# Performance work log

Measured on AMD Instinct MI355X. Metric: run time of the kernel, lower is better.

## Reference

```python
import jax, jax.numpy as jnp
import numpy as np

BS, DEG, H = 32, 4, 32
OUT = H  # n_aggr=1 inside Full -> out_size = n_aggr * h_size = h_size


def setup_inputs() -> dict:
    key = jax.random.key(0)
    k1, k2 = jax.random.split(key)
    neighbour_h = jax.random.normal(k1, (BS, DEG, H), dtype=jnp.float32)
    hp1 = H + 1
    t_shape = (hp1,) * DEG + (OUT,)  # [33,33,33,33,32]
    # xavier_uniform-like scale: fan_in = hp1**DEG, fan_out = OUT
    scale = float(np.sqrt(2.0 / (hp1 ** DEG + OUT)))
    T = jax.random.normal(k2, t_shape, dtype=jnp.float32) * scale
    return {"neighbour_h": neighbour_h, "T": T}


def reference(neighbour_h, T):
    # Full.forward: chunk neighbour_h along child dim, feed to AugmentedTensor.
    # AugmentedTensor: sequentially contract T against each child's augmented
    # embedding [h_i ; 1] over the leading axes of T.
    bs, deg, h = neighbour_h.shape
    hp1 = h + 1
    # augment with trailing 1 (bias slot): [bs, deg, h+1]
    h_aug = jnp.concatenate(
        [neighbour_h, jnp.ones((bs, deg, 1), neighbour_h.dtype)], axis=2
    )
    # first contraction: [bs, hp1] @ [hp1, hp1^(deg-1)*out]
    res = jnp.matmul(h_aug[:, 0, :], T.reshape(hp1, -1))
    # remaining contractions shrink the trailing dim by hp1 each step
    for i in range(1, deg):
        res = jnp.einsum("bi,bio->bo", h_aug[:, i, :], res.reshape(bs, hp1, -1))
    return res  # [bs, out_size] == [bs, h_size] since n_aggr=1
```

## Files before the change

### kernel.cpp

```cpp
#include <hip/hip_runtime.h>
#include <hip/hip_bf16.h>

#define HSZ 32
#define HP1 33
#define M3 35937
#define M3P2 35968
#define TI_STRIDE 1149984
#define TIB ((size_t)TI_STRIDE * 4)
#define NBLK 1124
#define NT 64
#define DEPTH 6

#define OFF_A0T   0
#define OFF_D     8192
#define OFF_TILES 4612096

typedef short bf16x8 __attribute__((ext_vector_type(8)));
typedef float f32x16 __attribute__((ext_vector_type(16)));

__device__ inline short f2bf(float f) {
  __hip_bfloat16 h = __float2bfloat16(f);
  return __builtin_bit_cast(short, h);
}

__global__ __launch_bounds__(256) void k_pre(const float* __restrict__ nh,
                                             float* __restrict__ a0T,
                                             float* __restrict__ D,
                                             float* __restrict__ tiles) {
  const int b = blockIdx.y;
  const int m = blockIdx.x * 256 + threadIdx.x;
  if (m < M3P2) {
    float v = 0.f;
    if (m < M3) {
      const int j = m / 1089;
      const int r = m - j * 1089;
      const int k = r / 33;
      const int l = r - k * 33;
      const float a1 = (j < HSZ) ? nh[(b * 4 + 1) * HSZ + j] : 1.0f;
      const float a2 = (k < HSZ) ? nh[(b * 4 + 2) * HSZ + k] : 1.0f;
      const float a3 = (l < HSZ) ? nh[(b * 4 + 3) * HSZ + l] : 1.0f;
      v = a1 * a2 * a3;
    }
    D[(size_t)b * M3P2 + m] = v;
  }
  if (blockIdx.x == 0 && threadIdx.x < HP1) {
    const int i = threadIdx.x;
    a0T[i * 32 + b] = (i < HSZ) ? nh[(b * 4 + 0) * HSZ + i] : 1.0f;
  }
  if (b == 1 && blockIdx.x < 64) {
    ((float4*)tiles)[blockIdx.x * 256 + threadIdx.x] =
        make_float4(0.f, 0.f, 0.f, 0.f);
  }
}

__global__ __launch_bounds__(64) void k_main(const float* __restrict__ T,
                                             const float* __restrict__ a0T,
                                             const float* __restrict__ D,
                                             float* __restrict__ tiles) {
  __shared__ float lds[DEPTH * 1024];
  const int blk = blockIdx.x;
  const int m0 = blk * 32;
  const int l = (int)threadIdx.x;
  const int bo = l & 31;
  const int g = l >> 5;

  const float* dp = D + (size_t)bo * M3P2 + m0 + 8 * g;
  float df0[8], df1[8];
  *(float4*)(df0)     = *(const float4*)(dp);
  *(float4*)(df0 + 4) = *(const float4*)(dp + 4);
  *(float4*)(df1)     = *(const float4*)(dp + 16);
  *(float4*)(df1 + 4) = *(const float4*)(dp + 20);

  float a0v[HP1];
#pragma unroll
  for (int i = 0; i < HP1; ++i) a0v[i] = a0T[i * 32 + bo];

  {
    float s = 0.f;
#pragma unroll
    for (int e = 0; e < 8; ++e) s += df0[e] + df1[e];
#pragma unroll
    for (int i = 0; i < HP1; ++i) s += a0v[i];
    asm volatile("" :: "v"(s) : "memory");
  }

  const int mrel = l >> 3;
  size_t src[4];
#pragma unroll
  for (int q = 0; q < 4; ++q) {
    const bool valid = (m0 + 8 * q + mrel) < M3;
    src[q] = valid ? ((size_t)(m0 * 32 + q * 256 + l * 4) * 4) : 0;
  }
  const char* Tb = (const char*)T;

#define ISSUE(row_, slot_)                                                    \
  {                                                                           \
    _Pragma("unroll")                                                         \
    for (int q = 0; q < 4; ++q) {                                             \
      __builtin_amdgcn_global_load_lds(                                       \
          (const __attribute__((address_space(1))) void*)(                    \
              Tb + (size_t)(row_)*TIB + src[q]),                              \
          (__attribute__((address_space(3))) void*)(                          \
              &lds[(slot_)*1024 + q * 256]),                                  \
          16, 0, 0);                                                          \
    }                                                                         \
  }

  ISSUE(0, 0) ISSUE(1, 1) ISSUE(2, 2) ISSUE(3, 3) ISSUE(4, 4) ISSUE(5, 5)

  f32x16 acc = {};

#define STEP(i_, vm_, doIssue_)                                               \
  {                                                                           \
    asm volatile("s_waitcnt vmcnt(" #vm_ ")" ::: "memory");                   \
    __builtin_amdgcn_sched_barrier(0);                                        \
    float tv0[8], tv1[8];                                                     \
    _Pragma("unroll")                                                         \
    for (int e = 0; e < 8; ++e) {                                             \
      tv0[e] = lds[((i_) % DEPTH) * 1024 + (8 * g + e) * 32 + bo];            \
      tv1[e] = lds[((i_) % DEPTH) * 1024 + 512 + (8 * g + e) * 32 + bo];      \
    }                                                                         \
    asm volatile("s_waitcnt lgkmcnt(0)" ::: "memory");                        \
    if (doIssue_) ISSUE((i_) + DEPTH, (i_) % DEPTH)                           \
    bf16x8 af0, bf0, af1, bf1;                                                \
    _Pragma("unroll")                                                         \
    for (int e = 0; e < 8; ++e) {                                             \
      af0[e] = f2bf(a0v[i_] * df0[e]);                                        \
      bf0[e] = f2bf(tv0[e]);                                                  \
      af1[e] = f2bf(a0v[i_] * df1[e]);                                        \
      bf1[e] = f2bf(tv1[e]);                                                  \
    }                                                                         \
    acc = __builtin_amdgcn_mfma_f32_32x32x16_bf16(af0, bf0, acc, 0, 0, 0);    \
    acc = __builtin_amdgcn_mfma_f32_32x32x16_bf16(af1, bf1, acc, 0, 0, 0);    \
  }

  STEP(0, 20, 1)  STEP(1, 20, 1)  STEP(2, 20, 1)  STEP(3, 20, 1)
  STEP(4, 20, 1)  STEP(5, 20, 1)  STEP(6, 20, 1)  STEP(7, 20, 1)
  STEP(8, 20, 1)  STEP(9, 20, 1)  STEP(10, 20, 1) STEP(11, 20, 1)
  STEP(12, 20, 1) STEP(13, 20, 1) STEP(14, 20, 1) STEP(15, 20, 1)
  STEP(16, 20, 1) STEP(17, 20, 1) STEP(18, 20, 1) STEP(19, 20, 1)
  STEP(20, 20, 1) STEP(21, 20, 1) STEP(22, 20, 1) STEP(23, 20, 1)
  STEP(24, 20, 1) STEP(25, 20, 1) STEP(26, 20, 1) STEP(27, 20, 0)
  STEP(28, 16, 0) STEP(29, 12, 0) STEP(30, 8, 0)  STEP(31, 4, 0)
  STEP(32, 0, 0)
#undef STEP
#undef ISSUE

  float* tp = tiles + (size_t)(blk & (NT - 1)) * 1024;
#pragma unroll
  for (int r = 0; r < 16; ++r) {
    const int brow = (r & 3) + 8 * (r >> 2) + 4 * g;
    atomicAdd(tp + brow * 32 + bo, acc[r]);
  }
}

__global__ __launch_bounds__(256) void k_red(const float* __restrict__ tiles,
                                             float* __restrict__ out) {
  const int idx = blockIdx.x * 256 + (int)threadIdx.x;
  float s = 0.f;
  for (int t = 0; t < NT; ++t) s += tiles[(size_t)t * 1024 + idx];
  out[idx] = s;
}

extern "C" void kernel_launch(void* const* d_in, const int* in_sizes, int n_in,
                              void* d_out, int out_size, void* d_ws, size_t ws_size,
                              hipStream_t stream) {
  const float* nh = (const float*)d_in[0];
  const float* T  = (const float*)d_in[1];
  float* out = (float*)d_out;
  char* ws = (char*)d_ws;
  float* a0T   = (float*)(ws + OFF_A0T);
  float* D     = (float*)(ws + OFF_D);
  float* tiles = (float*)(ws + OFF_TILES);

  k_pre<<<dim3(141, 32), 256, 0, stream>>>(nh, a0T, D, tiles);
  k_main<<<NBLK, 64, 0, stream>>>(T, a0T, D, tiles);
  k_red<<<4, 256, 0, stream>>>(tiles, out);
}
```

Measured before the change: 39.75 us.

## Compute outer-product factors in-kernel from LDS-staged transposed embeddings

The precompute kernel no longer materialises the large per-batch D tensor (32x35968 floats). It now only writes a small transposed, augmented copy of the embeddings (about 17 KB) and zeroes the tiles. The main kernel bulk-loads that copy into LDS, then builds its own a1*a2*a3 products and per-step a0 values from LDS. This removes a multi-megabyte global write and read plus a large pre-kernel launch grid, at the cost of extra integer division and LDS reads in every main block and a larger LDS footprint.

New measurement: 39.22 us. About the same (-1.3%).

```diff
diff --git a/kernel.cpp b/kernel.cpp
--- a/kernel.cpp
+++ b/kernel.cpp
@@ -4,16 +4,15 @@
 #define HSZ 32
 #define HP1 33
 #define M3 35937
-#define M3P2 35968
 #define TI_STRIDE 1149984
 #define TIB ((size_t)TI_STRIDE * 4)
 #define NBLK 1124
 #define NT 64
 #define DEPTH 6
+#define NHT 6144
+#define NHTG_FLOATS 4352
 
-#define OFF_A0T   0
-#define OFF_D     8192
-#define OFF_TILES 4612096
+#define OFF_TILES 32768
 
 typedef short bf16x8 __attribute__((ext_vector_type(8)));
 typedef float f32x16 __attribute__((ext_vector_type(16)));
@@ -24,65 +23,36 @@
 }
 
 __global__ __launch_bounds__(256) void k_pre(const float* __restrict__ nh,
-                                             float* __restrict__ a0T,
-                                             float* __restrict__ D,
+                                             float* __restrict__ nhTg,
                                              float* __restrict__ tiles) {
-  const int b = blockIdx.y;
-  const int m = blockIdx.x * 256 + threadIdx.x;
-  if (m < M3P2) {
-    float v = 0.f;
-    if (m < M3) {
-      const int j = m / 1089;
-      const int r = m - j * 1089;
-      const int k = r / 33;
-      const int l = r - k * 33;
-      const float a1 = (j < HSZ) ? nh[(b * 4 + 1) * HSZ + j] : 1.0f;
-      const float a2 = (k < HSZ) ? nh[(b * 4 + 2) * HSZ + k] : 1.0f;
-      const float a3 = (l < HSZ) ? nh[(b * 4 + 3) * HSZ + l] : 1.0f;
-      v = a1 * a2 * a3;
+  const int blk = (int)blockIdx.x;
+  const int t = (int)threadIdx.x;
+  if (blk < 64) {
+    ((float4*)tiles)[blk * 256 + t] = make_float4(0.f, 0.f, 0.f, 0.f);
+  } else {
+    for (int x = t; x < NHTG_FLOATS; x += 256) {
+      float v = 0.f;
+      if (x < 4224) {
+        const int d = x / 1056;
+        const int rem = x - d * 1056;
+        const int row = rem >> 5;
+        const int b = rem & 31;
+        v = (row < HSZ) ? nh[b * 128 + d * 32 + row] : 1.0f;
+      }
+      nhTg[x] = v;
     }
-    D[(size_t)b * M3P2 + m] = v;
-  }
-  if (blockIdx.x == 0 && threadIdx.x < HP1) {
-    const int i = threadIdx.x;
-    a0T[i * 32 + b] = (i < HSZ) ? nh[(b * 4 + 0) * HSZ + i] : 1.0f;
-  }
-  if (b == 1 && blockIdx.x < 64) {
-    ((float4*)tiles)[blockIdx.x * 256 + threadIdx.x] =
-        make_float4(0.f, 0.f, 0.f, 0.f);
   }
 }
 
 __global__ __launch_bounds__(64) void k_main(const float* __restrict__ T,
-                                             const float* __restrict__ a0T,
-                                             const float* __restrict__ D,
+                                             const float* __restrict__ nhTg,
                                              float* __restrict__ tiles) {
-  __shared__ float lds[DEPTH * 1024];
+  __shared__ float lds[DEPTH * 1024 + NHTG_FLOATS];
   const int blk = blockIdx.x;
   const int m0 = blk * 32;
   const int l = (int)threadIdx.x;
   const int bo = l & 31;
   const int g = l >> 5;
-
-  const float* dp = D + (size_t)bo * M3P2 + m0 + 8 * g;
-  float df0[8], df1[8];
-  *(float4*)(df0)     = *(const float4*)(dp);
-  *(float4*)(df0 + 4) = *(const float4*)(dp + 4);
-  *(float4*)(df1)     = *(const float4*)(dp + 16);
-  *(float4*)(df1 + 4) = *(const float4*)(dp + 20);
-
-  float a0v[HP1];
-#pragma unroll
-  for (int i = 0; i < HP1; ++i) a0v[i] = a0T[i * 32 + bo];
-
-  {
-    float s = 0.f;
-#pragma unroll
-    for (int e = 0; e < 8; ++e) s += df0[e] + df1[e];
-#pragma unroll
-    for (int i = 0; i < HP1; ++i) s += a0v[i];
-    asm volatile("" :: "v"(s) : "memory");
-  }
 
   const int mrel = l >> 3;
   size_t src[4];
@@ -92,6 +62,15 @@
     src[q] = valid ? ((size_t)(m0 * 32 + q * 256 + l * 4) * 4) : 0;
   }
   const char* Tb = (const char*)T;
+  const char* Ng = (const char*)nhTg;
+
+#pragma unroll
+  for (int q = 0; q < 17; ++q) {
+    __builtin_amdgcn_global_load_lds(
+        (const __attribute__((address_space(1))) void*)(Ng + q * 1024 + l * 16),
+        (__attribute__((address_space(3))) void*)(&lds[NHT + q * 256]),
+        16, 0, 0);
+  }
 
 #define ISSUE(row_, slot_)                                                    \
   {                                                                           \
@@ -108,6 +87,29 @@
 
   ISSUE(0, 0) ISSUE(1, 1) ISSUE(2, 2) ISSUE(3, 3) ISSUE(4, 4) ISSUE(5, 5)
 
+  asm volatile("s_waitcnt vmcnt(24)" ::: "memory");
+  __builtin_amdgcn_sched_barrier(0);
+
+  float df0[8], df1[8];
+#pragma unroll
+  for (int e = 0; e < 8; ++e) {
+#pragma unroll
+    for (int half = 0; half < 2; ++half) {
+      const int m = m0 + 16 * half + 8 * g + e;
+      const bool valid = m < M3;
+      const int mc = valid ? m : (M3 - 1);
+      const int j = mc / 1089;
+      const int r = mc - j * 1089;
+      const int kk = r / 33;
+      const int ll = r - kk * 33;
+      const float a1 = lds[NHT + 1056 + j * 32 + bo];
+      const float a2 = lds[NHT + 2112 + kk * 32 + bo];
+      const float a3 = lds[NHT + 3168 + ll * 32 + bo];
+      const float v = valid ? (a1 * a2 * a3) : 0.0f;
+      if (half == 0) df0[e] = v; else df1[e] = v;
+    }
+  }
+
   f32x16 acc = {};
 
 #define STEP(i_, vm_, doIssue_)                                               \
@@ -115,6 +117,7 @@
     asm volatile("s_waitcnt vmcnt(" #vm_ ")" ::: "memory");                   \
     __builtin_amdgcn_sched_barrier(0);                                        \
     float tv0[8], tv1[8];                                                     \
+    const float a0 = lds[NHT + (i_)*32 + bo];                                 \
     _Pragma("unroll")                                                         \
     for (int e = 0; e < 8; ++e) {                                             \
       tv0[e] = lds[((i_) % DEPTH) * 1024 + (8 * g + e) * 32 + bo];            \
@@ -125,9 +128,9 @@
     bf16x8 af0, bf0, af1, bf1;                                                \
     _Pragma("unroll")                                                         \
     for (int e = 0; e < 8; ++e) {                                             \
-      af0[e] = f2bf(a0v[i_] * df0[e]);                                        \
+      af0[e] = f2bf(a0 * df0[e]);                                             \
       bf0[e] = f2bf(tv0[e]);                                                  \
-      af1[e] = f2bf(a0v[i_] * df1[e]);                                        \
+      af1[e] = f2bf(a0 * df1[e]);                                             \
       bf1[e] = f2bf(tv1[e]);                                                  \
     }                                                                         \
     acc = __builtin_amdgcn_mfma_f32_32x32x16_bf16(af0, bf0, acc, 0, 0, 0);    \
@@ -169,11 +172,10 @@
   const float* T  = (const float*)d_in[1];
   float* out = (float*)d_out;
   char* ws = (char*)d_ws;
-  float* a0T   = (float*)(ws + OFF_A0T);
-  float* D     = (float*)(ws + OFF_D);
+  float* nhTg  = (float*)ws;
   float* tiles = (float*)(ws + OFF_TILES);
 
-  k_pre<<<dim3(141, 32), 256, 0, stream>>>(nh, a0T, D, tiles);
-  k_main<<<NBLK, 64, 0, stream>>>(T, a0T, D, tiles);
+  k_pre<<<65, 256, 0, stream>>>(nh, nhTg, tiles);
+  k_main<<<NBLK, 64, 0, stream>>>(T, nhTg, tiles);
   k_red<<<4, 256, 0, stream>>>(tiles, out);
 }
```
